# Performance work log

Hardware: AMD Instinct MI355X
Metric: run time of the kernel (lower is better)

The kernel has to match this reference:

```python
import jax, jax.numpy as jnp
import numpy as np

D_MODEL = 1024
N_HEAD = 16
SEG = 256
HEAD_DIM = D_MODEL // N_HEAD  # 64; only used as softmax scale (module never splits heads)
SCALE = 1.0 / (HEAD_DIM ** 0.5)


def setup_inputs() -> dict:
    key = jax.random.key(0)
    ks = jax.random.split(key, 9)
    B, L, D = 4, 4096, D_MODEL
    s = 1.0 / np.sqrt(D)
    x = jax.random.normal(ks[0], (B, L, D), dtype=jnp.float32)
    Wq = jax.random.uniform(ks[1], (D, D), jnp.float32, -s, s)
    bq = jax.random.uniform(ks[2], (D,), jnp.float32, -s, s)
    Wk = jax.random.uniform(ks[3], (D, D), jnp.float32, -s, s)
    bk = jax.random.uniform(ks[4], (D,), jnp.float32, -s, s)
    Wv = jax.random.uniform(ks[5], (D, D), jnp.float32, -s, s)
    bv = jax.random.uniform(ks[6], (D,), jnp.float32, -s, s)
    Wo = jax.random.uniform(ks[7], (D, D), jnp.float32, -s, s)
    bo = jax.random.uniform(ks[8], (D,), jnp.float32, -s, s)
    return {"x": x, "Wq": Wq, "bq": bq, "Wk": Wk, "bk": bk,
            "Wv": Wv, "bv": bv, "Wo": Wo, "bo": bo}


def reference(x, Wq, bq, Wk, bk, Wv, bv, Wo, bo):
    B, L, D = x.shape
    n_seg = L // SEG
    xs = x.reshape(B, n_seg, SEG, D)  # [B, n, S, D] block-diagonal segments

    # Local (per-segment) attention, batched over all segments at once.
    Q = jnp.einsum('bnsd,ed->bnse', xs, Wq) + bq
    K = jnp.einsum('bnsd,ed->bnse', xs, Wk) + bk
    V = jnp.einsum('bnsd,ed->bnse', xs, Wv) + bv
    scores = jnp.einsum('bnse,bnte->bnst', Q, K) * SCALE  # [B, n, S, S]
    attn = jax.nn.softmax(scores, axis=-1)
    local = jnp.einsum('bnst,bnte->bnse', attn, V)  # [B, n, S, D]

    # Global attention over segment summaries (first token of each segment).
    summ = xs[:, :, 0, :]  # [B, n, D]
    Qg = jnp.einsum('bnd,ed->bne', summ, Wq) + bq
    Kg = jnp.einsum('bnd,ed->bne', summ, Wk) + bk
    Vg = jnp.einsum('bnd,ed->bne', summ, Wv) + bv
    scores_g = jnp.einsum('bne,bme->bnm', Qg, Kg) * SCALE  # [B, n, n]
    attn_g = jax.nn.softmax(scores_g, axis=-1)
    global_out = jnp.einsum('bnm,bme->bne', attn_g, Vg)  # [B, n, D]

    # Broadcast each segment's global summary over its tokens and add.
    out = local + global_out[:, :, None, :]  # [B, n, S, D]
    out = out.reshape(B, L, D)
    return jnp.einsum('bld,ed->ble', out, Wo) + bo
```

## Files before the change

kernel.cpp:

```cpp
#include <hip/hip_runtime.h>
#include <hip/hip_bf16.h>
#include <stdint.h>

typedef unsigned short u16;
typedef __attribute__((ext_vector_type(8))) short s16x8;
typedef __attribute__((ext_vector_type(4))) short s16x4;
typedef __attribute__((ext_vector_type(4))) float f32x4;

__device__ __forceinline__ u16 f2bf(float f){
  uint32_t u = __builtin_bit_cast(uint32_t, f);
  u += 0x7FFFu + ((u >> 16) & 1u);
  return (u16)(u >> 16);
}
__device__ __forceinline__ float bf2f(u16 h){
  uint32_t u = ((uint32_t)h) << 16;
  return __builtin_bit_cast(float, u);
}
__device__ __forceinline__ void gl_lds16(const void* g, void* l){
  __builtin_amdgcn_global_load_lds((__attribute__((address_space(1))) void*)g,
                                   (__attribute__((address_space(3))) void*)l,
                                   16, 0, 0);
}

#define MROWS 16384
#define DMODEL 1024
#define NQKV 3072
#define NSEGS 64
#define O_XB    0u
#define O_WQKV  33554432u
#define O_WO    39845888u
#define O_BQKV  41943040u
#define O_QKV   41955328u
#define O_VT    142618624u
#define O_GOUT  176173056u
#define O_GPR   176435200u

__global__ __launch_bounds__(256) void pack_kernel(
    const float* __restrict__ x,
    const float* __restrict__ wq, const float* __restrict__ wk,
    const float* __restrict__ wv, const float* __restrict__ wo,
    const float* __restrict__ bq, const float* __restrict__ bk, const float* __restrict__ bv,
    u16* __restrict__ xb, u16* __restrict__ wqkvb, u16* __restrict__ wob,
    float* __restrict__ bqkv)
{
  const int stride = gridDim.x * 256;
  const int gid = blockIdx.x * 256 + threadIdx.x;
  if(gid < 3072)
    bqkv[gid] = (gid < 1024) ? bq[gid] : (gid < 2048 ? bk[gid - 1024] : bv[gid - 2048]);
  for(int q = gid; q < 4194304; q += stride){
    float4 v = *(const float4*)(x + (size_t)q * 4);
    ushort4 o; o.x = f2bf(v.x); o.y = f2bf(v.y); o.z = f2bf(v.z); o.w = f2bf(v.w);
    *(ushort4*)(xb + (size_t)q * 4) = o;
  }
  for(int q = gid; q < 786432; q += stride){
    int elem = q << 2;
    int m = elem >> 20;
    const float* s = (m == 0) ? wq : (m == 1 ? wk : wv);
    float4 v = *(const float4*)(s + (elem & 1048575));
    ushort4 o; o.x = f2bf(v.x); o.y = f2bf(v.y); o.z = f2bf(v.z); o.w = f2bf(v.w);
    *(ushort4*)(wqkvb + elem) = o;
  }
  for(int q = gid; q < 262144; q += stride){
    float4 v = *(const float4*)(wo + (size_t)q * 4);
    ushort4 o; o.x = f2bf(v.x); o.y = f2bf(v.y); o.z = f2bf(v.z); o.w = f2bf(v.w);
    *(ushort4*)(wob + (size_t)q * 4) = o;
  }
}

__global__ __launch_bounds__(512, 2) void gemm256_kernel(
    const u16* __restrict__ A, const u16* __restrict__ Bt,
    const float* __restrict__ bias, u16* __restrict__ Cv,
    u16* __restrict__ Vt, const int K, const int ldc, const int ncb)
{
  __shared__ char sm[131072];
  const int tid = threadIdx.x;
  const int wv = tid >> 6, lane = tid & 63;
  const int l15 = lane & 15, l4 = lane >> 4;
  const int wr = wv >> 2, wc = wv & 3;

  const int nwg = (int)gridDim.x;
  int bid = (int)blockIdx.x;
  bid = (bid & 7) * (nwg >> 3) + (bid >> 3);
  const int brow = (bid / ncb) << 8, bcol = (bid % ncb) << 8;

  int offA[8], offB[4];
#pragma unroll
  for(int m = 0; m < 8; ++m){
    int row = wr * 128 + m * 16 + l15;
    offA[m] = row * 64 + ((l4 ^ ((row >> 1) & 3)) << 4);
  }
#pragma unroll
  for(int n = 0; n < 4; ++n){
    int row = wc * 64 + n * 16 + l15;
    offB[n] = 16384 + row * 64 + ((l4 ^ ((row >> 1) & 3)) << 4);
  }

  const u16* srcA[2]; const u16* srcB[2]; int dstOff[2];
#pragma unroll
  for(int r = 0; r < 2; ++r){
    int off = r * 8192 + tid * 16;
    int row = off >> 6, g = (off >> 4) & 3;
    int gs = g ^ ((row >> 1) & 3);
    srcA[r] = A  + (size_t)(brow + row) * K + gs * 8;
    srcB[r] = Bt + (size_t)(bcol + row) * K + gs * 8;
    dstOff[r] = r * 8192 + wv * 1024;
  }

#define STAGE256(kt_, buf_) do{                                   \
    char* base_ = sm + (buf_) * 32768;                            \
    const int ko_ = (kt_) << 5;                                   \
    gl_lds16(srcA[0] + ko_, base_ + dstOff[0]);                   \
    gl_lds16(srcA[1] + ko_, base_ + dstOff[1]);                   \
    gl_lds16(srcB[0] + ko_, base_ + 16384 + dstOff[0]);           \
    gl_lds16(srcB[1] + ko_, base_ + 16384 + dstOff[1]);           \
  }while(0)

  const f32x4 fz = {0.f, 0.f, 0.f, 0.f};
  f32x4 acc[8][4];
#pragma unroll
  for(int m = 0; m < 8; ++m)
#pragma unroll
    for(int n = 0; n < 4; ++n) acc[m][n] = fz;

  const int nkt = K >> 5;
  STAGE256(0, 0); STAGE256(1, 1); STAGE256(2, 2);

  for(int kt = 0; kt < nkt; ++kt){
    const int rem = nkt - 1 - kt;
    if(rem >= 2)      asm volatile("s_waitcnt vmcnt(8)" ::: "memory");
    else if(rem == 1) asm volatile("s_waitcnt vmcnt(4)" ::: "memory");
    else              asm volatile("s_waitcnt vmcnt(0)" ::: "memory");
    __builtin_amdgcn_s_barrier();
    asm volatile("" ::: "memory");
    if(kt + 3 < nkt) STAGE256(kt + 3, (kt + 3) & 3);

    char* cb = sm + (kt & 3) * 32768;
    s16x8 b[4], a[4];
#pragma unroll
    for(int n = 0; n < 4; ++n) b[n] = *(const s16x8*)(cb + offB[n]);
#pragma unroll
    for(int m = 0; m < 4; ++m) a[m] = *(const s16x8*)(cb + offA[m]);
    __builtin_amdgcn_s_setprio(1);
#pragma unroll
    for(int m = 0; m < 4; ++m)
#pragma unroll
      for(int n = 0; n < 4; ++n)
        acc[m][n] = __builtin_amdgcn_mfma_f32_16x16x32_bf16(a[m], b[n], acc[m][n], 0, 0, 0);
    __builtin_amdgcn_s_setprio(0);
#pragma unroll
    for(int m = 0; m < 4; ++m) a[m] = *(const s16x8*)(cb + offA[m + 4]);
    __builtin_amdgcn_s_setprio(1);
#pragma unroll
    for(int m = 0; m < 4; ++m)
#pragma unroll
      for(int n = 0; n < 4; ++n)
        acc[m + 4][n] = __builtin_amdgcn_mfma_f32_16x16x32_bf16(a[m], b[n], acc[m + 4][n], 0, 0, 0);
    __builtin_amdgcn_s_setprio(0);
  }
#undef STAGE256

  float bvv[4];
#pragma unroll
  for(int n = 0; n < 4; ++n) bvv[n] = bias[bcol + wc * 64 + n * 16 + l15];
#pragma unroll
  for(int m = 0; m < 8; ++m)
#pragma unroll
    for(int n = 0; n < 4; ++n)
#pragma unroll
      for(int r = 0; r < 4; ++r){
        const int row = brow + wr * 128 + m * 16 + (l4 << 2) + r;
        const int col = bcol + wc * 64 + n * 16 + l15;
        Cv[(size_t)row * ldc + col] = f2bf(acc[m][n][r] + bvv[n]);
      }

  if(bcol >= 2048){
    __syncthreads();
    char* wbase = sm + wv * 16384;
    const int swzW = (l15 & 7) << 4;
#pragma unroll
    for(int n = 0; n < 4; ++n)
#pragma unroll
      for(int m = 0; m < 8; ++m){
        s16x4 pk;
#pragma unroll
        for(int r = 0; r < 4; ++r) pk[r] = (short)f2bf(acc[m][n][r] + bvv[n]);
        const int eL = n * 16 + l15;
        const int tB = (m * 16 + (l4 << 2)) * 2;
        *(s16x4*)(wbase + ((eL * 256 + tB) ^ swzW)) = pk;
      }
    asm volatile("s_waitcnt lgkmcnt(0)" ::: "memory");
    const int seg = brow >> 8;
    const int e0  = bcol - 2048 + wc * 64;
    const int c = lane & 15, eSub = lane >> 4;
#pragma unroll
    for(int i = 0; i < 16; ++i){
      const int eL = i * 4 + eSub;
      s16x8 vvv = *(const s16x8*)(wbase + ((eL * 256 + c * 16) ^ ((eL & 7) << 4)));
      *(s16x8*)(Vt + (size_t)seg * 262144 + (size_t)(e0 + eL) * 256 + wr * 128 + c * 8) = vvv;
    }
  }
}

__global__ __launch_bounds__(512, 4) void gemm128_kernel(
    const u16* __restrict__ A, const u16* __restrict__ Bt,
    const float* __restrict__ bias, float* __restrict__ C,
    const int K, const int ldc, const int ncb)
{
  __shared__ char sm[73728];
  const int tid = threadIdx.x;
  const int wv = tid >> 6, lane = tid & 63;
  const int l15 = lane & 15, l4 = lane >> 4;
  const int wr = wv >> 2, wc = wv & 3;

  const int nwg = (int)gridDim.x;
  int bid = (int)blockIdx.x;
  bid = (bid & 7) * (nwg >> 3) + (bid >> 3);
  const int brow = (bid / ncb) << 8, bcol = (bid % ncb) << 7;

  int offA[8], offB[2];
#pragma unroll
  for(int m = 0; m < 8; ++m){
    int row = wr * 128 + m * 16 + l15;
    offA[m] = row * 64 + ((l4 ^ ((row >> 1) & 3)) << 4);
  }
#pragma unroll
  for(int n = 0; n < 2; ++n){
    int row = wc * 32 + n * 16 + l15;
    offB[n] = 16384 + row * 64 + ((l4 ^ ((row >> 1) & 3)) << 4);
  }

  const u16* srcA[2]; const u16* srcB; int dstOff[2];
#pragma unroll
  for(int r = 0; r < 2; ++r){
    int off = r * 8192 + tid * 16;
    int row = off >> 6, g = (off >> 4) & 3;
    int gs = g ^ ((row >> 1) & 3);
    srcA[r] = A + (size_t)(brow + row) * K + gs * 8;
    dstOff[r] = r * 8192 + wv * 1024;
  }
  {
    int off = tid * 16;
    int row = off >> 6, g = (off >> 4) & 3;
    int gs = g ^ ((row >> 1) & 3);
    srcB = Bt + (size_t)(bcol + row) * K + gs * 8;
  }

#define STAGE128(kt_, buf_) do{                                   \
    char* base_ = sm + (buf_) * 24576;                            \
    const int ko_ = (kt_) << 5;                                   \
    gl_lds16(srcA[0] + ko_, base_ + dstOff[0]);                   \
    gl_lds16(srcA[1] + ko_, base_ + dstOff[1]);                   \
    gl_lds16(srcB + ko_, base_ + 16384 + wv * 1024);              \
  }while(0)

  const f32x4 fz = {0.f, 0.f, 0.f, 0.f};
  f32x4 acc[8][2];
#pragma unroll
  for(int m = 0; m < 8; ++m)
#pragma unroll
    for(int n = 0; n < 2; ++n) acc[m][n] = fz;

  const int nkt = K >> 5;
  STAGE128(0, 0); STAGE128(1, 1);
  int cur = 0;
  for(int kt = 0; kt < nkt; ++kt){
    if(kt + 1 < nkt) asm volatile("s_waitcnt vmcnt(3)" ::: "memory");
    else             asm volatile("s_waitcnt vmcnt(0)" ::: "memory");
    __builtin_amdgcn_s_barrier();
    asm volatile("" ::: "memory");
    if(kt + 2 < nkt){
      int nb = cur + 2; if(nb >= 3) nb -= 3;
      STAGE128(kt + 2, nb);
    }
    char* cb = sm + cur * 24576;
    s16x8 b[2], a[4];
#pragma unroll
    for(int n = 0; n < 2; ++n) b[n] = *(const s16x8*)(cb + offB[n]);
#pragma unroll
    for(int m = 0; m < 4; ++m) a[m] = *(const s16x8*)(cb + offA[m]);
    __builtin_amdgcn_s_setprio(1);
#pragma unroll
    for(int m = 0; m < 4; ++m)
#pragma unroll
      for(int n = 0; n < 2; ++n)
        acc[m][n] = __builtin_amdgcn_mfma_f32_16x16x32_bf16(a[m], b[n], acc[m][n], 0, 0, 0);
    __builtin_amdgcn_s_setprio(0);
#pragma unroll
    for(int m = 0; m < 4; ++m) a[m] = *(const s16x8*)(cb + offA[m + 4]);
    __builtin_amdgcn_s_setprio(1);
#pragma unroll
    for(int m = 0; m < 4; ++m)
#pragma unroll
      for(int n = 0; n < 2; ++n)
        acc[m + 4][n] = __builtin_amdgcn_mfma_f32_16x16x32_bf16(a[m], b[n], acc[m + 4][n], 0, 0, 0);
    __builtin_amdgcn_s_setprio(0);
    if(++cur == 3) cur = 0;
  }
#undef STAGE128

  float bvv[2];
#pragma unroll
  for(int n = 0; n < 2; ++n) bvv[n] = bias[bcol + wc * 32 + n * 16 + l15];
#pragma unroll
  for(int m = 0; m < 8; ++m)
#pragma unroll
    for(int n = 0; n < 2; ++n)
#pragma unroll
      for(int r = 0; r < 4; ++r){
        const int row = brow + wr * 128 + m * 16 + (l4 << 2) + r;
        const int col = bcol + wc * 32 + n * 16 + l15;
        C[(size_t)row * ldc + col] = acc[m][n][r] + bvv[n];
      }
}

__global__ __launch_bounds__(256) void gscore_kernel(
    const u16* __restrict__ QKV, float* __restrict__ gpr)
{
  __shared__ float sc[16];
  const int b = blockIdx.x >> 4, i = blockIdx.x & 15;
  const int tid = threadIdx.x;
  const int j = tid >> 4, slice = tid & 15;
  const u16* qp = QKV + (size_t)(b * 16 + i) * 256 * NQKV + slice * 64;
  const u16* kp = QKV + (size_t)(b * 16 + j) * 256 * NQKV + 1024 + slice * 64;
  float acc = 0.f;
#pragma unroll
  for(int c = 0; c < 8; ++c){
    s16x8 qv = *(const s16x8*)(qp + c * 8);
    s16x8 kv = *(const s16x8*)(kp + c * 8);
#pragma unroll
    for(int e = 0; e < 8; ++e) acc += bf2f((u16)qv[e]) * bf2f((u16)kv[e]);
  }
#pragma unroll
  for(int off = 8; off >= 1; off >>= 1) acc += __shfl_xor(acc, off, 64);
  if(slice == 0) sc[j] = acc * 0.125f;
  __syncthreads();
  if(tid < 16){
    float v = sc[tid];
    float m = v;
#pragma unroll
    for(int off = 8; off >= 1; off >>= 1) m = fmaxf(m, __shfl_xor(m, off, 64));
    float p = __expf(v - m);
    float s = p;
#pragma unroll
    for(int off = 8; off >= 1; off >>= 1) s += __shfl_xor(s, off, 64);
    gpr[(size_t)b * 256 + i * 16 + tid] = p / s;
  }
}

__global__ __launch_bounds__(256) void gpv_kernel(
    const u16* __restrict__ QKV, const float* __restrict__ gpr,
    float* __restrict__ gout)
{
  __shared__ float spr[256];
  const int b = blockIdx.x >> 4, ch = blockIdx.x & 15;
  const int tid = threadIdx.x;
  spr[tid] = gpr[(size_t)b * 256 + tid];
  __syncthreads();
  const int e = (ch << 6) + (tid & 63);
  const int ng = tid >> 6;
  const u16* vp = QKV + (size_t)(b * 16) * 256 * NQKV + 2048 + e;
  float o0 = 0.f, o1 = 0.f, o2 = 0.f, o3 = 0.f;
#pragma unroll
  for(int m = 0; m < 16; ++m){
    float v = bf2f(vp[(size_t)m * 256 * NQKV]);
    o0 += spr[(ng * 4 + 0) * 16 + m] * v;
    o1 += spr[(ng * 4 + 1) * 16 + m] * v;
    o2 += spr[(ng * 4 + 2) * 16 + m] * v;
    o3 += spr[(ng * 4 + 3) * 16 + m] * v;
  }
  gout[((size_t)b * 16 + ng * 4 + 0) * 1024 + e] = o0;
  gout[((size_t)b * 16 + ng * 4 + 1) * 1024 + e] = o1;
  gout[((size_t)b * 16 + ng * 4 + 2) * 1024 + e] = o2;
  gout[((size_t)b * 16 + ng * 4 + 3) * 1024 + e] = o3;
}

__global__ __launch_bounds__(512, 2) void attn_local_kernel(
    const u16* __restrict__ QKV, const u16* __restrict__ Vt,
    const float* __restrict__ gout, u16* __restrict__ AO)
{
  __shared__ char sm[131072];
  float* smax = (float*)(sm + 32768);
  float* ssum = (float*)(sm + 33792);
  const int tid = threadIdx.x;
  const int wv = tid >> 6, lane = tid & 63;
  const int l15 = lane & 15, l4 = lane >> 4;
  const int wr = wv >> 2, wc = wv & 3;
  int bid = (int)blockIdx.x;
  bid = (bid & 7) * 32 + (bid >> 3);
  const int seg = bid >> 2, rt = bid & 3;
  const int r0 = rt << 6;
  const size_t segQ = (size_t)seg * 256 * NQKV;

  const int offq = wv * 1024 + lane * 16;
  const int dstQ = wv * 1024;
  const int qrow = offq >> 7;
  const int qgs  = ((offq >> 4) & 7) ^ (qrow & 7);
  const u16* qsrc = QKV + segQ + (size_t)(r0 + qrow) * NQKV + qgs * 8;
  const u16* ksrc[4];
  const u16* vsrc[4];
#pragma unroll
  for(int c = 0; c < 4; ++c){
    int off = c * 8192 + offq;
    int row = off >> 7;
    int gs  = ((off >> 4) & 7) ^ (row & 7);
    ksrc[c] = QKV + segQ + (size_t)row * NQKV + 1024 + gs * 8;
    vsrc[c] = Vt + (size_t)seg * 262144 + (size_t)row * 256 + gs * 8;
  }

#define STAGE_P1(d0_, base_) do{                                        \
    gl_lds16(qsrc + (d0_), sm + (base_) + dstQ);                        \
    _Pragma("unroll")                                                   \
    for(int c_ = 0; c_ < 4; ++c_)                                       \
      gl_lds16(ksrc[c_] + (d0_), sm + (base_) + 8192 + c_ * 8192 + dstQ); \
  }while(0)
#define STAGE_V(j_, vb_) do{                                            \
    const int vo_ = ((j_) >> 2) * 65536 + ((j_) & 3) * 64;              \
    _Pragma("unroll")                                                   \
    for(int c_ = 0; c_ < 4; ++c_)                                       \
      gl_lds16(vsrc[c_] + vo_, sm + 32768 + (vb_) * 32768 + c_ * 8192 + dstQ); \
  }while(0)

  int aOff[2][2], bOff[4][2];
#pragma unroll
  for(int m = 0; m < 2; ++m){
    int row = wr * 32 + m * 16 + l15;
#pragma unroll
    for(int kk = 0; kk < 2; ++kk)
      aOff[m][kk] = row * 128 + ((kk * 64 + l4 * 16) ^ ((row & 7) << 4));
  }
#pragma unroll
  for(int n = 0; n < 4; ++n){
    int row = wc * 64 + n * 16 + l15;
#pragma unroll
    for(int kk = 0; kk < 2; ++kk)
      bOff[n][kk] = 8192 + row * 128 + ((kk * 64 + l4 * 16) ^ ((row & 7) << 4));
  }

  const f32x4 fz = {0.f, 0.f, 0.f, 0.f};
  f32x4 acc1[2][4];
#pragma unroll
  for(int m = 0; m < 2; ++m)
#pragma unroll
    for(int n = 0; n < 4; ++n) acc1[m][n] = fz;

  STAGE_P1(0, 0); STAGE_P1(64, 40960);
  asm volatile("s_waitcnt vmcnt(5)" ::: "memory");
  __builtin_amdgcn_s_barrier();
  asm volatile("" ::: "memory");
  int cur = 0;
  for(int dt = 0; dt < 16; ++dt){
    const int base = cur * 40960;
    if(dt + 2 < 16){
      int nb = cur + 2; if(nb >= 3) nb -= 3;
      STAGE_P1((dt + 2) << 6, nb * 40960);
    }
    s16x8 a[2][2], b[4][2];
#pragma unroll
    for(int m = 0; m < 2; ++m)
#pragma unroll
      for(int kk = 0; kk < 2; ++kk) a[m][kk] = *(const s16x8*)(sm + base + aOff[m][kk]);
#pragma unroll
    for(int n = 0; n < 4; ++n)
#pragma unroll
      for(int kk = 0; kk < 2; ++kk) b[n][kk] = *(const s16x8*)(sm + base + bOff[n][kk]);
    __builtin_amdgcn_s_setprio(1);
#pragma unroll
    for(int kk = 0; kk < 2; ++kk)
#pragma unroll
      for(int m = 0; m < 2; ++m)
#pragma unroll
        for(int n = 0; n < 4; ++n)
          acc1[m][n] = __builtin_amdgcn_mfma_f32_16x16x32_bf16(a[m][kk], b[n][kk], acc1[m][n], 0, 0, 0);
    __builtin_amdgcn_s_setprio(0);
    if(dt + 2 < 16) asm volatile("s_waitcnt vmcnt(5) lgkmcnt(0)" ::: "memory");
    else            asm volatile("s_waitcnt vmcnt(0) lgkmcnt(0)" ::: "memory");
    __builtin_amdgcn_s_barrier();
    asm volatile("" ::: "memory");
    if(++cur == 3) cur = 0;
  }

  const float CE = 0.18033688011112042f;
#pragma unroll
  for(int m = 0; m < 2; ++m)
#pragma unroll
    for(int r = 0; r < 4; ++r){
      float v = -1e30f;
#pragma unroll
      for(int n = 0; n < 4; ++n) v = fmaxf(v, acc1[m][n][r]);
#pragma unroll
      for(int off = 8; off >= 1; off >>= 1) v = fmaxf(v, __shfl_xor(v, off, 64));
      if(l15 == 0) smax[wc * 64 + wr * 32 + m * 16 + (l4 << 2) + r] = v;
    }
  asm volatile("s_waitcnt lgkmcnt(0)" ::: "memory");
  __builtin_amdgcn_s_barrier();
  asm volatile("" ::: "memory");
#pragma unroll
  for(int m = 0; m < 2; ++m)
#pragma unroll
    for(int r = 0; r < 4; ++r){
      const int idx = wr * 32 + m * 16 + (l4 << 2) + r;
      const float g = fmaxf(fmaxf(smax[idx], smax[64 + idx]),
                            fmaxf(smax[128 + idx], smax[192 + idx]));
      float s = 0.f;
#pragma unroll
      for(int n = 0; n < 4; ++n){
        float p = exp2f((acc1[m][n][r] - g) * CE);
        acc1[m][n][r] = p;
        s += p;
      }
#pragma unroll
      for(int off = 8; off >= 1; off >>= 1) s += __shfl_xor(s, off, 64);
      if(l15 == 0) ssum[wc * 64 + idx] = s;
    }
  asm volatile("s_waitcnt lgkmcnt(0)" ::: "memory");
  __builtin_amdgcn_s_barrier();
  asm volatile("" ::: "memory");
  float inv2[2][4];
#pragma unroll
  for(int m = 0; m < 2; ++m)
#pragma unroll
    for(int r = 0; r < 4; ++r){
      const int idx = wr * 32 + m * 16 + (l4 << 2) + r;
      inv2[m][r] = 1.f / (ssum[idx] + ssum[64 + idx] + ssum[128 + idx] + ssum[192 + idx]);
    }
#pragma unroll
  for(int m = 0; m < 2; ++m)
#pragma unroll
    for(int n = 0; n < 4; ++n)
#pragma unroll
      for(int r = 0; r < 4; ++r){
        const int rr = wr * 32 + m * 16 + (l4 << 2) + r;
        const int t  = wc * 64 + n * 16 + l15;
        *(u16*)(sm + rr * 512 + ((t << 1) ^ ((rr & 7) << 4))) = f2bf(acc1[m][n][r] * inv2[m][r]);
      }
  asm volatile("s_waitcnt lgkmcnt(0)" ::: "memory");
  __builtin_amdgcn_s_barrier();
  asm volatile("" ::: "memory");

  int prow[2], pswz[2];
#pragma unroll
  for(int m = 0; m < 2; ++m){
    int row = wr * 32 + m * 16 + l15;
    prow[m] = row * 512;
    pswz[m] = (row & 7) << 4;
  }
  int vOff[4][2];
#pragma unroll
  for(int n = 0; n < 4; ++n){
    int row = wc * 64 + n * 16 + l15;
#pragma unroll
    for(int kk = 0; kk < 2; ++kk)
      vOff[n][kk] = row * 128 + ((kk * 64 + l4 * 16) ^ ((row & 7) << 4));
  }

  STAGE_V(0, 0); STAGE_V(1, 1);
  asm volatile("s_waitcnt vmcnt(4)" ::: "memory");
  __builtin_amdgcn_s_barrier();
  asm volatile("" ::: "memory");
  f32x4 acc2[2][4];
  int cv = 0;
  for(int j = 0; j < 16; ++j){
    const int ts = j & 3, ns = j >> 2;
    if(ts == 0){
#pragma unroll
      for(int m = 0; m < 2; ++m)
#pragma unroll
        for(int n = 0; n < 4; ++n) acc2[m][n] = fz;
    }
    if(j + 2 < 16){
      int nb = cv + 2; if(nb >= 3) nb -= 3;
      STAGE_V(j + 2, nb);
    }
    char* vbase = sm + 32768 + cv * 32768;
    s16x8 a[2][2], b[4][2];
#pragma unroll
    for(int m = 0; m < 2; ++m)
#pragma unroll
      for(int kk = 0; kk < 2; ++kk)
        a[m][kk] = *(const s16x8*)(sm + prow[m] + (((ts << 7) + (kk << 6) + (l4 << 4)) ^ pswz[m]));
#pragma unroll
    for(int n = 0; n < 4; ++n)
#pragma unroll
      for(int kk = 0; kk < 2; ++kk) b[n][kk] = *(const s16x8*)(vbase + vOff[n][kk]);
    __builtin_amdgcn_s_setprio(1);
#pragma unroll
    for(int kk = 0; kk < 2; ++kk)
#pragma unroll
      for(int m = 0; m < 2; ++m)
#pragma unroll
        for(int n = 0; n < 4; ++n)
          acc2[m][n] = __builtin_amdgcn_mfma_f32_16x16x32_bf16(a[m][kk], b[n][kk], acc2[m][n], 0, 0, 0);
    __builtin_amdgcn_s_setprio(0);
    if(j + 2 < 16) asm volatile("s_waitcnt vmcnt(4) lgkmcnt(0)" ::: "memory");
    else           asm volatile("s_waitcnt vmcnt(0) lgkmcnt(0)" ::: "memory");
    __builtin_amdgcn_s_barrier();
    asm volatile("" ::: "memory");
    if(++cv == 3) cv = 0;

    if(ts == 3){
      float gv[4];
#pragma unroll
      for(int n = 0; n < 4; ++n)
        gv[n] = gout[(size_t)seg * 1024 + ns * 256 + wc * 64 + n * 16 + l15];
#pragma unroll
      for(int m = 0; m < 2; ++m)
#pragma unroll
        for(int n = 0; n < 4; ++n)
#pragma unroll
          for(int r = 0; r < 4; ++r){
            const int row = r0 + wr * 32 + m * 16 + (l4 << 2) + r;
            const int e   = ns * 256 + wc * 64 + n * 16 + l15;
            AO[((size_t)seg * 256 + row) * 1024 + e] = f2bf(acc2[m][n][r] + gv[n]);
          }
    }
  }
#undef STAGE_P1
#undef STAGE_V
}

extern "C" void kernel_launch(void* const* d_in, const int* in_sizes, int n_in,
                              void* d_out, int out_size, void* d_ws, size_t ws_size,
                              hipStream_t stream)
{
  const float* x  = (const float*)d_in[0];
  const float* Wq = (const float*)d_in[1];
  const float* bq = (const float*)d_in[2];
  const float* Wk = (const float*)d_in[3];
  const float* bk = (const float*)d_in[4];
  const float* Wv = (const float*)d_in[5];
  const float* bv = (const float*)d_in[6];
  const float* Wo = (const float*)d_in[7];
  const float* bo = (const float*)d_in[8];

  char* ws = (char*)d_ws;
  u16*   xb    = (u16*)(ws + O_XB);
  u16*   wqkvb = (u16*)(ws + O_WQKV);
  u16*   wob   = (u16*)(ws + O_WO);
  float* bqkv  = (float*)(ws + O_BQKV);
  u16*   qkv   = (u16*)(ws + O_QKV);
  u16*   vt    = (u16*)(ws + O_VT);
  float* gout  = (float*)(ws + O_GOUT);
  float* gpr   = (float*)(ws + O_GPR);
  u16*   ao    = xb;

  pack_kernel<<<4096, 256, 0, stream>>>(x, Wq, Wk, Wv, Wo, bq, bk, bv, xb, wqkvb, wob, bqkv);
  gemm256_kernel<<<dim3((NQKV / 256) * (MROWS / 256)), 512, 0, stream>>>(
      xb, wqkvb, bqkv, qkv, vt, DMODEL, NQKV, NQKV / 256);
  gscore_kernel<<<64, 256, 0, stream>>>(qkv, gpr);
  gpv_kernel<<<64, 256, 0, stream>>>(qkv, gpr, gout);
  attn_local_kernel<<<256, 512, 0, stream>>>(qkv, vt, gout, ao);
  gemm128_kernel<<<dim3((DMODEL / 128) * (MROWS / 256)), 512, 0, stream>>>(
      ao, wob, bo, (float*)d_out, DMODEL, DMODEL, DMODEL / 128);
}
```

Measured before the change: 223.9 us.

## Shrink QKV GEMM tile to 128x128 and skip writing V to row-major buffer

The QKV projection GEMM moves from a 256x256 tile with 512 threads to a 128x128 tile with 256 threads and 64KB of LDS. This gives four times as many workgroups for better CU fill, at the cost of less operand reuse per tile. V columns are now written only in the transposed Vt layout, not also into the row-major QKV buffer, which cuts redundant global stores. The global PV kernel is updated to read V from Vt.

```diff
diff --git a/kernel.cpp b/kernel.cpp
--- a/kernel.cpp
+++ b/kernel.cpp
@@ -67,63 +67,62 @@
   }
 }
 
-__global__ __launch_bounds__(512, 2) void gemm256_kernel(
+__global__ __launch_bounds__(256, 2) void gemm_qkv_kernel(
     const u16* __restrict__ A, const u16* __restrict__ Bt,
-    const float* __restrict__ bias, u16* __restrict__ Cv,
-    u16* __restrict__ Vt, const int K, const int ldc, const int ncb)
+    const float* __restrict__ bias, u16* __restrict__ Cv, u16* __restrict__ Vt)
 {
-  __shared__ char sm[131072];
+  __shared__ char sm[65536];
   const int tid = threadIdx.x;
   const int wv = tid >> 6, lane = tid & 63;
   const int l15 = lane & 15, l4 = lane >> 4;
-  const int wr = wv >> 2, wc = wv & 3;
+  const int wr = wv >> 1, wc = wv & 1;
 
   const int nwg = (int)gridDim.x;
   int bid = (int)blockIdx.x;
   bid = (bid & 7) * (nwg >> 3) + (bid >> 3);
-  const int brow = (bid / ncb) << 8, bcol = (bid % ncb) << 8;
-
-  int offA[8], offB[4];
-#pragma unroll
-  for(int m = 0; m < 8; ++m){
-    int row = wr * 128 + m * 16 + l15;
+  const int brow = (bid / 24) << 7, bcol = (bid % 24) << 7;
+
+  int offA[4], offB[4];
+#pragma unroll
+  for(int m = 0; m < 4; ++m){
+    int row = wr * 64 + m * 16 + l15;
     offA[m] = row * 64 + ((l4 ^ ((row >> 1) & 3)) << 4);
   }
 #pragma unroll
   for(int n = 0; n < 4; ++n){
     int row = wc * 64 + n * 16 + l15;
-    offB[n] = 16384 + row * 64 + ((l4 ^ ((row >> 1) & 3)) << 4);
+    offB[n] = 8192 + row * 64 + ((l4 ^ ((row >> 1) & 3)) << 4);
   }
 
   const u16* srcA[2]; const u16* srcB[2]; int dstOff[2];
 #pragma unroll
   for(int r = 0; r < 2; ++r){
-    int off = r * 8192 + tid * 16;
+    int off = r * 4096 + tid * 16;
     int row = off >> 6, g = (off >> 4) & 3;
     int gs = g ^ ((row >> 1) & 3);
-    srcA[r] = A  + (size_t)(brow + row) * K + gs * 8;
-    srcB[r] = Bt + (size_t)(bcol + row) * K + gs * 8;
-    dstOff[r] = r * 8192 + wv * 1024;
-  }
-
-#define STAGE256(kt_, buf_) do{                                   \
-    char* base_ = sm + (buf_) * 32768;                            \
+    srcA[r] = A  + (size_t)(brow + row) * 1024 + gs * 8;
+    srcB[r] = Bt + (size_t)(bcol + row) * 1024 + gs * 8;
+    dstOff[r] = r * 4096 + wv * 1024;
+  }
+
+#define STAGEQ(kt_, buf_) do{                                     \
+    char* base_ = sm + (buf_) * 16384;                            \
     const int ko_ = (kt_) << 5;                                   \
     gl_lds16(srcA[0] + ko_, base_ + dstOff[0]);                   \
     gl_lds16(srcA[1] + ko_, base_ + dstOff[1]);                   \
-    gl_lds16(srcB[0] + ko_, base_ + 16384 + dstOff[0]);           \
-    gl_lds16(srcB[1] + ko_, base_ + 16384 + dstOff[1]);           \
+    gl_lds16(srcB[0] + ko_, base_ + 8192 + dstOff[0]);            \
+    gl_lds16(srcB[1] + ko_, base_ + 8192 + dstOff[1]);            \
   }while(0)
 
   const f32x4 fz = {0.f, 0.f, 0.f, 0.f};
-  f32x4 acc[8][4];
-#pragma unroll
-  for(int m = 0; m < 8; ++m)
+  f32x4 acc[4][4];
+#pragma unroll
+  for(int m = 0; m < 4; ++m)
 #pragma unroll
     for(int n = 0; n < 4; ++n) acc[m][n] = fz;
 
-  const int nkt = K >> 5;
-  STAGE256(0, 0); STAGE256(1, 1); STAGE256(2, 2);
+  const int nkt = 32;
+  STAGEQ(0, 0); STAGEQ(1, 1); STAGEQ(2, 2);
 
   for(int kt = 0; kt < nkt; ++kt){
     const int rem = nkt - 1 - kt;
@@ -132,9 +131,9 @@
     else              asm volatile("s_waitcnt vmcnt(0)" ::: "memory");
     __builtin_amdgcn_s_barrier();
     asm volatile("" ::: "memory");
-    if(kt + 3 < nkt) STAGE256(kt + 3, (kt + 3) & 3);
-
-    char* cb = sm + (kt & 3) * 32768;
+    if(kt + 3 < nkt) STAGEQ(kt + 3, (kt + 3) & 3);
+
+    char* cb = sm + (kt & 3) * 16384;
     s16x8 b[4], a[4];
 #pragma unroll
     for(int n = 0; n < 4; ++n) b[n] = *(const s16x8*)(cb + offB[n]);
@@ -147,56 +146,49 @@
       for(int n = 0; n < 4; ++n)
         acc[m][n] = __builtin_amdgcn_mfma_f32_16x16x32_bf16(a[m], b[n], acc[m][n], 0, 0, 0);
     __builtin_amdgcn_s_setprio(0);
-#pragma unroll
-    for(int m = 0; m < 4; ++m) a[m] = *(const s16x8*)(cb + offA[m + 4]);
-    __builtin_amdgcn_s_setprio(1);
+  }
+#undef STAGEQ
+
+  float bvv[4];
+#pragma unroll
+  for(int n = 0; n < 4; ++n) bvv[n] = bias[bcol + wc * 64 + n * 16 + l15];
+
+  if(bcol < 2048){
 #pragma unroll
     for(int m = 0; m < 4; ++m)
 #pragma unroll
       for(int n = 0; n < 4; ++n)
-        acc[m + 4][n] = __builtin_amdgcn_mfma_f32_16x16x32_bf16(a[m], b[n], acc[m + 4][n], 0, 0, 0);
-    __builtin_amdgcn_s_setprio(0);
-  }
-#undef STAGE256
-
-  float bvv[4];
-#pragma unroll
-  for(int n = 0; n < 4; ++n) bvv[n] = bias[bcol + wc * 64 + n * 16 + l15];
-#pragma unroll
-  for(int m = 0; m < 8; ++m)
+#pragma unroll
+        for(int r = 0; r < 4; ++r){
+          const int row = brow + wr * 64 + m * 16 + (l4 << 2) + r;
+          const int col = bcol + wc * 64 + n * 16 + l15;
+          Cv[(size_t)row * NQKV + col] = f2bf(acc[m][n][r] + bvv[n]);
+        }
+  } else {
+    __syncthreads();
+    char* wbase = sm + wv * 8192;
+    const int swzW = (l15 & 7) << 4;
 #pragma unroll
     for(int n = 0; n < 4; ++n)
 #pragma unroll
-      for(int r = 0; r < 4; ++r){
-        const int row = brow + wr * 128 + m * 16 + (l4 << 2) + r;
-        const int col = bcol + wc * 64 + n * 16 + l15;
-        Cv[(size_t)row * ldc + col] = f2bf(acc[m][n][r] + bvv[n]);
-      }
-
-  if(bcol >= 2048){
-    __syncthreads();
-    char* wbase = sm + wv * 16384;
-    const int swzW = (l15 & 7) << 4;
-#pragma unroll
-    for(int n = 0; n < 4; ++n)
-#pragma unroll
-      for(int m = 0; m < 8; ++m){
+      for(int m = 0; m < 4; ++m){
         s16x4 pk;
 #pragma unroll
         for(int r = 0; r < 4; ++r) pk[r] = (short)f2bf(acc[m][n][r] + bvv[n]);
         const int eL = n * 16 + l15;
         const int tB = (m * 16 + (l4 << 2)) * 2;
-        *(s16x4*)(wbase + ((eL * 256 + tB) ^ swzW)) = pk;
+        *(s16x4*)(wbase + ((eL * 128 + tB) ^ swzW)) = pk;
       }
     asm volatile("s_waitcnt lgkmcnt(0)" ::: "memory");
     const int seg = brow >> 8;
+    const int t0  = (brow & 255) + wr * 64;
     const int e0  = bcol - 2048 + wc * 64;
-    const int c = lane & 15, eSub = lane >> 4;
-#pragma unroll
-    for(int i = 0; i < 16; ++i){
-      const int eL = i * 4 + eSub;
-      s16x8 vvv = *(const s16x8*)(wbase + ((eL * 256 + c * 16) ^ ((eL & 7) << 4)));
-      *(s16x8*)(Vt + (size_t)seg * 262144 + (size_t)(e0 + eL) * 256 + wr * 128 + c * 8) = vvv;
+    const int c = lane & 7, eSub = lane >> 3;
+#pragma unroll
+    for(int i = 0; i < 8; ++i){
+      const int eL = i * 8 + eSub;
+      s16x8 vvv = *(const s16x8*)(wbase + ((eL * 128 + c * 16) ^ ((eL & 7) << 4)));
+      *(s16x8*)(Vt + (size_t)seg * 262144 + (size_t)(e0 + eL) * 256 + t0 + c * 8) = vvv;
     }
   }
 }
@@ -348,7 +340,7 @@
 }
 
 __global__ __launch_bounds__(256) void gpv_kernel(
-    const u16* __restrict__ QKV, const float* __restrict__ gpr,
+    const u16* __restrict__ Vt, const float* __restrict__ gpr,
     float* __restrict__ gout)
 {
   __shared__ float spr[256];
@@ -358,11 +350,11 @@
   __syncthreads();
   const int e = (ch << 6) + (tid & 63);
   const int ng = tid >> 6;
-  const u16* vp = QKV + (size_t)(b * 16) * 256 * NQKV + 2048 + e;
+  const u16* vp = Vt + (size_t)(b * 16) * 262144 + (size_t)e * 256;
   float o0 = 0.f, o1 = 0.f, o2 = 0.f, o3 = 0.f;
 #pragma unroll
   for(int m = 0; m < 16; ++m){
-    float v = bf2f(vp[(size_t)m * 256 * NQKV]);
+    float v = bf2f(vp[(size_t)m * 262144]);
     o0 += spr[(ng * 4 + 0) * 16 + m] * v;
     o1 += spr[(ng * 4 + 1) * 16 + m] * v;
     o2 += spr[(ng * 4 + 2) * 16 + m] * v;
@@ -644,10 +636,10 @@
   u16*   ao    = xb;
 
   pack_kernel<<<4096, 256, 0, stream>>>(x, Wq, Wk, Wv, Wo, bq, bk, bv, xb, wqkvb, wob, bqkv);
-  gemm256_kernel<<<dim3((NQKV / 256) * (MROWS / 256)), 512, 0, stream>>>(
-      xb, wqkvb, bqkv, qkv, vt, DMODEL, NQKV, NQKV / 256);
+  gemm_qkv_kernel<<<dim3((NQKV / 128) * (MROWS / 128)), 256, 0, stream>>>(
+      xb, wqkvb, bqkv, qkv, vt);
   gscore_kernel<<<64, 256, 0, stream>>>(qkv, gpr);
-  gpv_kernel<<<64, 256, 0, stream>>>(qkv, gpr, gout);
+  gpv_kernel<<<64, 256, 0, stream>>>(vt, gpr, gout);
   attn_local_kernel<<<256, 512, 0, stream>>>(qkv, vt, gout, ao);
   gemm128_kernel<<<dim3((DMODEL / 128) * (MROWS / 256)), 512, 0, stream>>>(
       ao, wob, bo, (float*)d_out, DMODEL, DMODEL, DMODEL / 128);
```

Result: slower. 243.4 us (+8.7%).
